# Kernel tuning notes

Measured on AMD Instinct MI355X. Metric: run time of the kernel, lower is better.

The kernel has to match this reference:

```python
import jax, jax.numpy as jnp
import numpy as np

B, L, HID, NH, E = 2, 2048, 1024, 16, 128
HS = HID // NH  # attention_head_size = 64 (scores scaled by sqrt(HS), NOT sqrt(E))


def setup_inputs() -> dict:
    key = jax.random.key(0)
    ks = jax.random.split(key, 8)
    s = 0.02
    return {
        "hidden_states": jax.random.normal(ks[0], (B, L, HID), jnp.float32),
        "attention_mask": jnp.zeros((B, 1, 1, L), jnp.float32),
        "rel_pos": jax.random.normal(ks[1], (1, NH, L, L), jnp.float32),
        "Wq": jax.random.normal(ks[2], (NH * E, HID), jnp.float32) * s,
        "bq": jnp.zeros((NH * E,), jnp.float32),
        "Wk": jax.random.normal(ks[3], (NH * E, HID), jnp.float32) * s,
        "Wv": jax.random.normal(ks[4], (HID, HID), jnp.float32) * s,
        "bv": jnp.zeros((HID,), jnp.float32),
        "Wg": jax.random.normal(ks[5], (8, E), jnp.float32) * s,
        "bg": jnp.zeros((8,), jnp.float32),
        "eco_a": jnp.ones((1, NH, 1, 1), jnp.float32),
    }


def reference(hidden_states, attention_mask, rel_pos, Wq, bq, Wk, Wv, bv, Wg, bg, eco_a):
    b, l, _ = hidden_states.shape
    # projections -> [B, H, L, E] / [B, H, L, HS]
    q = (hidden_states @ Wq.T + bq).reshape(b, l, NH, E).transpose(0, 2, 1, 3)
    k = (hidden_states @ Wk.T).reshape(b, l, NH, E).transpose(0, 2, 1, 3)
    v = (hidden_states @ Wv.T + bv).reshape(b, l, NH, HS).transpose(0, 2, 1, 3)
    scores = jnp.einsum('bhqe,bhke->bhqk', q, k) / jnp.asarray(np.sqrt(HS), q.dtype)
    scores = scores + attention_mask
    # gated relative-position bias: gate_ur_linear(q) -> [B,H,L,2,4] -> sum -> sigmoid
    g = jax.nn.sigmoid((q @ Wg.T + bg).reshape(b, NH, l, 2, 4).sum(-1))
    gate_u, gate_r = g[..., 0:1], g[..., 1:2]  # each [B,H,L,1]
    gate_u_1 = gate_u * (gate_r * eco_a - 1.0) + 2.0
    scores = scores + gate_u_1 * rel_pos
    probs = jax.nn.softmax(scores, axis=-1)  # dropout p=0 -> identity
    ctx = jnp.einsum('bhqk,bhkd->bhqd', probs, v)
    return ctx.transpose(0, 2, 1, 3).reshape(b, l, HID)
```

## Files before the change

### kernel.cpp

```cpp
#include <hip/hip_runtime.h>
#include <hip/hip_bf16.h>
#include <stdint.h>

#define Bn 2
#define Ln 2048
#define HIDn 1024
#define NHn 16
#define En 128
#define HSn 64

typedef unsigned short u16;
typedef short s16x8 __attribute__((ext_vector_type(8)));
typedef float f32x4 __attribute__((ext_vector_type(4)));
typedef float f32x16 __attribute__((ext_vector_type(16)));

__device__ __forceinline__ u16 f2bf(float f) {
  union { float f; uint32_t u; } v; v.f = f;
  uint32_t r = (v.u + 0x7fffu + ((v.u >> 16) & 1u)) >> 16;
  return (u16)r;
}
__device__ __forceinline__ float bf2f(u16 b) {
  union { uint32_t u; float f; } v; v.u = ((uint32_t)b) << 16;
  return v.f;
}
__device__ __forceinline__ void async16(const void* g, void* l) {
  __builtin_amdgcn_global_load_lds((const __attribute__((address_space(1))) void*)g,
                                   (__attribute__((address_space(3))) void*)l, 16, 0, 0);
}

__global__ void castbf(const float* __restrict__ in, u16* __restrict__ out, int n) {
  int i = (blockIdx.x * blockDim.x + threadIdx.x) * 4;
  if (i >= n) return;
  float4 v = *(const float4*)(in + i);
  u16 o[4] = {f2bf(v.x), f2bf(v.y), f2bf(v.z), f2bf(v.w)};
  *(uint64_t*)(out + i) = *(uint64_t*)o;
}

__global__ void wgprep(const float* __restrict__ Wg, float* __restrict__ wgu,
                       float* __restrict__ wgr) {
  int e = threadIdx.x;
  wgu[e] = Wg[0 * 128 + e] + Wg[1 * 128 + e] + Wg[2 * 128 + e] + Wg[3 * 128 + e];
  wgr[e] = Wg[4 * 128 + e] + Wg[5 * 128 + e] + Wg[6 * 128 + e] + Wg[7 * 128 + e];
}

__global__ __launch_bounds__(256) void qkv_gemm(
    const u16* __restrict__ A, const u16* __restrict__ W,
    const float* __restrict__ bq, const float* __restrict__ bv,
    u16* __restrict__ qb, u16* __restrict__ kb, u16* __restrict__ vt) {
  __shared__ union {
    struct { u16 a[128 * 32]; u16 b[128 * 32]; } st;
    u16 cq[64][140];
    u16 cv[128][72];
  } lds;
  const int tid = threadIdx.x, lane = tid & 63, w = tid >> 6;
  const int quad = lane >> 4, ln = lane & 15;
  const int bx = blockIdx.x, by = blockIdx.y;
  const int m0 = (w >> 1) * 64, n0 = (w & 1) * 64;
  f32x4 acc[4][4];
  for (int i = 0; i < 4; ++i)
    for (int j = 0; j < 4; ++j) acc[i][j] = (f32x4)0.0f;

  for (int k0 = 0; k0 < 1024; k0 += 32) {
    __syncthreads();
    for (int cc = 0; cc < 2; ++cc) {
      int c = w * 2 + cc;
      int row = c * 16 + (lane >> 2);
      int ke = (lane & 3) * 8;
      async16(A + (size_t)(by * 128 + row) * 1024 + k0 + ke, lds.st.a + c * 512);
      async16(W + (size_t)(bx * 128 + row) * 1024 + k0 + ke, lds.st.b + c * 512);
    }
    __syncthreads();
    s16x8 a[4], bf[4];
    for (int i = 0; i < 4; ++i)
      a[i] = *(const s16x8*)&lds.st.a[(m0 + i * 16 + ln) * 32 + quad * 8];
    for (int j = 0; j < 4; ++j)
      bf[j] = *(const s16x8*)&lds.st.b[(n0 + j * 16 + ln) * 32 + quad * 8];
    for (int i = 0; i < 4; ++i)
      for (int j = 0; j < 4; ++j)
        acc[i][j] = __builtin_amdgcn_mfma_f32_16x16x32_bf16(a[i], bf[j], acc[i][j], 0, 0, 0);
  }

  float bias[4];
#pragma unroll
  for (int j = 0; j < 4; ++j) {
    int col = bx * 128 + n0 + j * 16 + ln;
    bias[j] = (bx < 16) ? bq[col] : (bx >= 32 ? bv[col - 4096] : 0.0f);
  }

  if (bx < 32) {
    for (int half = 0; half < 2; ++half) {
      __syncthreads();
      if ((w >> 1) == half) {
#pragma unroll
        for (int i = 0; i < 4; ++i)
#pragma unroll
          for (int j = 0; j < 4; ++j)
#pragma unroll
            for (int r = 0; r < 4; ++r)
              lds.cq[i * 16 + quad * 4 + r][n0 + j * 16 + ln] = f2bf(acc[i][j][r] + bias[j]);
      }
      __syncthreads();
#pragma unroll
      for (int it = 0; it < 4; ++it) {
        int slot = it * 256 + tid;
        int row = slot >> 4, seg = slot & 15;
        int rowg = by * 128 + half * 64 + row;
        int b = rowg >> 11, l = rowg & 2047;
        uint4 d = *(const uint4*)&lds.cq[row][seg * 8];
        if (bx < 16) {
          *(uint4*)(qb + ((size_t)(b * 16 + bx) * 2048 + l) * 128 + seg * 8) = d;
        } else {
          int sg = (seg ^ (l & 15)) & 15;
          *(uint4*)(kb + ((size_t)(b * 16 + (bx - 16)) * 2048 + l) * 128 + sg * 8) = d;
        }
      }
    }
  } else {
    for (int half = 0; half < 2; ++half) {
      __syncthreads();
      if ((w >> 1) == half) {
#pragma unroll
        for (int i = 0; i < 4; ++i)
#pragma unroll
          for (int j = 0; j < 4; ++j)
#pragma unroll
            for (int r = 0; r < 4; ++r)
              lds.cv[n0 + j * 16 + ln][i * 16 + quad * 4 + r] = f2bf(acc[i][j][r] + bias[j]);
      }
      __syncthreads();
      int rowg = by * 128 + half * 64;
      int b = rowg >> 11, lbase = rowg & 2047;
#pragma unroll
      for (int it = 0; it < 4; ++it) {
        int slot = it * 256 + tid;
        int row = slot >> 3, seg = slot & 7;
        int c2 = (bx - 32) * 128 + row;
        int h = c2 >> 6, hs = c2 & 63;
        int sg = seg ^ (hs & 7);
        uint4 d = *(const uint4*)&lds.cv[row][seg * 8];
        *(uint4*)(vt + ((size_t)(b * 16 + h) * 64 + hs) * 2048 + lbase + sg * 8) = d;
      }
    }
  }
}

__global__ void gate_kernel(const u16* __restrict__ qb, const float* __restrict__ wgu,
                            const float* __restrict__ wgr, const float* __restrict__ bg,
                            const float* __restrict__ eco, float* __restrict__ gate) {
  int t = blockIdx.x * 256 + threadIdx.x;
  int h = (t >> 11) & 15;
  const u16* q = qb + (size_t)t * 128;
  float u = bg[0] + bg[1] + bg[2] + bg[3];
  float rr = bg[4] + bg[5] + bg[6] + bg[7];
  for (int e = 0; e < 128; e += 8) {
    uint4 d = *(const uint4*)(q + e);
    const u16* p = (const u16*)&d;
#pragma unroll
    for (int jj = 0; jj < 8; ++jj) {
      float f = bf2f(p[jj]);
      u += f * wgu[e + jj];
      rr += f * wgr[e + jj];
    }
  }
  float gu = 1.0f / (1.0f + __expf(-u));
  float gr = 1.0f / (1.0f + __expf(-rr));
  gate[t] = gu * (gr * eco[h] - 1.0f) + 2.0f;
}

__global__ __launch_bounds__(256, 2) void attn_kernel(
    const u16* __restrict__ qb, const u16* __restrict__ kbp, const u16* __restrict__ vt,
    const float* __restrict__ mask, const float* __restrict__ relpos,
    const float* __restrict__ gate, float* __restrict__ out) {
  __shared__ u16 sK[2][64 * 128];
  __shared__ u16 sVt[2][64 * 64];
  __shared__ float sRP[128 * 64];

  const int tid = threadIdx.x, lane = tid & 63, w = tid >> 6;
  const int q5 = lane & 31, hi = lane >> 5;
  const int bx = blockIdx.x, h = blockIdx.y;
  const int qt = bx >> 1, b = bx & 1;
  const int q0 = qt * 128;
  const u16* qptr = qb + (size_t)(b * NHn + h) * Ln * En;
  const u16* kptr = kbp + (size_t)(b * NHn + h) * Ln * En;
  const u16* vptr = vt + (size_t)(b * NHn + h) * HSn * Ln;
  const float* rpb = relpos + (size_t)h * Ln * Ln + (size_t)q0 * Ln;
  const float* mk = mask + (size_t)b * Ln;
  const float* gt = gate + (size_t)(b * NHn + h) * Ln;

  s16x8 aq[8];
  {
    const u16* qrow = qptr + (size_t)(q0 + w * 32 + q5) * En;
#pragma unroll
    for (int es = 0; es < 8; ++es)
      aq[es] = *(const s16x8*)(qrow + es * 16 + hi * 8);
  }
  const float gv = gt[q0 + w * 32 + q5];

  float l_part = 0.0f;
  f32x16 O0 = (f32x16)0.0f, O1 = (f32x16)0.0f;

  auto stage = [&](int buf, int kt) {
    const int kbase = kt * 64;
#pragma unroll
    for (int cc = 0; cc < 4; ++cc) {
      int c = w * 4 + cc;
      async16(kptr + (size_t)(kbase + c * 4 + (lane >> 4)) * En + (lane & 15) * 8,
              &sK[buf][c * 512]);
    }
#pragma unroll
    for (int cc = 0; cc < 2; ++cc) {
      int c = w * 2 + cc;
      async16(vptr + (size_t)(c * 8 + (lane >> 3)) * Ln + kbase + (lane & 7) * 8,
              &sVt[buf][c * 512]);
    }
  };
  auto rpload = [&](int kt, float4 (&rg)[8]) {
#pragma unroll
    for (int i = 0; i < 8; ++i) {
      int s = i * 256 + tid;
      int qq = s >> 4, gc = s & 15;
      rg[i] = *(const float4*)(rpb + (size_t)qq * Ln + kt * 64 + gc * 4);
    }
  };
  auto rpwrite = [&](const float4 (&rg)[8]) {
#pragma unroll
    for (int i = 0; i < 8; ++i) {
      int s = i * 256 + tid;
      int qq = s >> 4, gc = s & 15;
      *(float4*)&sRP[qq * 64 + ((gc ^ (qq & 15)) * 4)] = rg[i];
    }
  };

  const int NT = Ln / 64;
  stage(0, 0);
  float4 rg[8];
  rpload(0, rg);
  rpwrite(rg);

  for (int kt = 0; kt < NT; ++kt) {
    const int cur = kt & 1;
    __syncthreads();
    if (kt + 1 < NT) {
      stage(cur ^ 1, kt + 1);
      rpload(kt + 1, rg);
    }

    const u16* sKc = sK[cur];
    f32x16 S0 = (f32x16)0.0f, S1 = (f32x16)0.0f;
    __builtin_amdgcn_s_setprio(1);
#pragma unroll
    for (int es = 0; es < 8; ++es) {
      int gsw = ((es * 2 + hi) ^ (q5 & 15)) * 8;
      s16x8 ak0 = *(const s16x8*)&sKc[q5 * 128 + gsw];
      S0 = __builtin_amdgcn_mfma_f32_32x32x16_bf16(ak0, aq[es], S0, 0, 0, 0);
      s16x8 ak1 = *(const s16x8*)&sKc[(32 + q5) * 128 + gsw];
      S1 = __builtin_amdgcn_mfma_f32_32x32x16_bf16(ak1, aq[es], S1, 0, 0, 0);
    }
    __builtin_amdgcn_s_setprio(0);

    uint32_t pkv[16];
#pragma unroll
    for (int kbi = 0; kbi < 2; ++kbi) {
      const f32x16 Sa = kbi ? S1 : S0;
#pragma unroll
      for (int g = 0; g < 4; ++g) {
        f32x4 rp4 = *(const f32x4*)&sRP[(w * 32 + q5) * 64 +
                                        (((kbi * 8 + g * 2 + hi) ^ (q5 & 15)) * 4)];
        float4 mv4 = *(const float4*)(mk + kt * 64 + kbi * 32 + g * 8 + hi * 4);
        float p0 = __expf(fmaf(gv, rp4[0], fmaf(Sa[4 * g + 0], 0.125f, mv4.x)));
        float p1 = __expf(fmaf(gv, rp4[1], fmaf(Sa[4 * g + 1], 0.125f, mv4.y)));
        float p2 = __expf(fmaf(gv, rp4[2], fmaf(Sa[4 * g + 2], 0.125f, mv4.z)));
        float p3 = __expf(fmaf(gv, rp4[3], fmaf(Sa[4 * g + 3], 0.125f, mv4.w)));
        l_part += (p0 + p1) + (p2 + p3);
        uint32_t c0, c1;
        asm("v_cvt_pk_bf16_f32 %0, %1, %2" : "=v"(c0) : "v"(p0), "v"(p1));
        asm("v_cvt_pk_bf16_f32 %0, %1, %2" : "=v"(c1) : "v"(p2), "v"(p3));
        pkv[kbi * 8 + g * 2] = c0;
        pkv[kbi * 8 + g * 2 + 1] = c1;
      }
    }
#pragma unroll
    for (int base = 0; base < 16; base += 8) {
      asm volatile("v_permlane32_swap_b32 %0, %1" : "+v"(pkv[base + 0]), "+v"(pkv[base + 2]));
      asm volatile("v_permlane32_swap_b32 %0, %1" : "+v"(pkv[base + 1]), "+v"(pkv[base + 3]));
      asm volatile("v_permlane32_swap_b32 %0, %1" : "+v"(pkv[base + 4]), "+v"(pkv[base + 6]));
      asm volatile("v_permlane32_swap_b32 %0, %1" : "+v"(pkv[base + 5]), "+v"(pkv[base + 7]));
    }

    if (kt + 1 < NT) {
#pragma unroll
      for (int i = 0; i < 8; ++i)
        asm volatile("" : "+v"(rg[i].x), "+v"(rg[i].y), "+v"(rg[i].z), "+v"(rg[i].w));
    }
    __syncthreads();
    if (kt + 1 < NT) rpwrite(rg);

    const u16* sVc = sVt[cur];
    __builtin_amdgcn_s_setprio(1);
#pragma unroll
    for (int ks2 = 0; ks2 < 4; ++ks2) {
      union { uint32_t u[4]; s16x8 v; } pu;
      pu.u[0] = pkv[ks2 * 4 + 0];
      pu.u[1] = pkv[ks2 * 4 + 1];
      pu.u[2] = pkv[ks2 * 4 + 2];
      pu.u[3] = pkv[ks2 * 4 + 3];
      s16x8 pa = pu.v;
      int gsw = ((ks2 * 2 + hi) ^ (q5 & 7)) * 8;
      s16x8 bv0 = *(const s16x8*)&sVc[q5 * 64 + gsw];
      O0 = __builtin_amdgcn_mfma_f32_32x32x16_bf16(pa, bv0, O0, 0, 0, 0);
      s16x8 bv1 = *(const s16x8*)&sVc[(32 + q5) * 64 + gsw];
      O1 = __builtin_amdgcn_mfma_f32_32x32x16_bf16(pa, bv1, O1, 0, 0, 0);
    }
    __builtin_amdgcn_s_setprio(0);
  }

  float lt = l_part + __shfl_xor(l_part, 32, 64);
  float inv = 1.0f / lt;
#pragma unroll
  for (int i = 0; i < 16; ++i) {
    int qr = (i & 3) + 8 * (i >> 2) + 4 * hi;
    float iv = __shfl(inv, qr, 64);
    int qg = q0 + w * 32 + qr;
    float* orow = out + ((size_t)b * Ln + qg) * HIDn + h * 64;
    orow[q5] = O0[i] * iv;
    orow[32 + q5] = O1[i] * iv;
  }
}

extern "C" void kernel_launch(void* const* d_in, const int* in_sizes, int n_in,
                              void* d_out, int out_size, void* d_ws, size_t ws_size,
                              hipStream_t stream) {
  const float* hs = (const float*)d_in[0];
  const float* mask = (const float*)d_in[1];
  const float* relpos = (const float*)d_in[2];
  const float* Wq = (const float*)d_in[3];
  const float* bq = (const float*)d_in[4];
  const float* Wk = (const float*)d_in[5];
  const float* Wv = (const float*)d_in[6];
  const float* bv = (const float*)d_in[7];
  const float* Wg = (const float*)d_in[8];
  const float* bg = (const float*)d_in[9];
  const float* eco = (const float*)d_in[10];
  float* out = (float*)d_out;

  char* ws = (char*)d_ws;
  u16* hsb = (u16*)ws;
  u16* wb = (u16*)(ws + (8ull << 20));
  u16* qb = (u16*)(ws + (18ull << 20));
  u16* kb = (u16*)(ws + (34ull << 20));
  u16* vt = (u16*)(ws + (50ull << 20));
  float* gate = (float*)(ws + (58ull << 20));
  float* wgu = (float*)(ws + (58ull << 20) + (1ull << 19));
  float* wgr = wgu + 128;

  castbf<<<4096, 256, 0, stream>>>(hs, hsb, 4096 * 1024);
  castbf<<<2048, 256, 0, stream>>>(Wq, wb, 2048 * 1024);
  castbf<<<2048, 256, 0, stream>>>(Wk, wb + 2048 * 1024, 2048 * 1024);
  castbf<<<1024, 256, 0, stream>>>(Wv, wb + 4096 * 1024, 1024 * 1024);
  wgprep<<<1, 128, 0, stream>>>(Wg, wgu, wgr);
  qkv_gemm<<<dim3(40, 32), 256, 0, stream>>>(hsb, wb, bq, bv, qb, kb, vt);
  gate_kernel<<<256, 256, 0, stream>>>(qb, wgu, wgr, bg, eco, gate);
  attn_kernel<<<dim3(32, 16), 256, 0, stream>>>(qb, kb, vt, mask, relpos, gate, out);
}
```

Before: 551.0 us.

## Deepen K/V and rel_pos prefetch pipeline with explicit vmcnt waits and barriers

```diff
diff --git a/kernel.cpp b/kernel.cpp
--- a/kernel.cpp
+++ b/kernel.cpp
@@ -232,18 +232,17 @@
   };
 
   const int NT = Ln / 64;
-  stage(0, 0);
+  float mcons = mk[lane];
   float4 rg[8];
   rpload(0, rg);
+  stage(0, 0);
   rpwrite(rg);
+  rpload(1, rg);
+  stage(1, 1);
+  asm volatile("s_waitcnt vmcnt(14) lgkmcnt(0)\n\ts_barrier" ::: "memory");
 
   for (int kt = 0; kt < NT; ++kt) {
     const int cur = kt & 1;
-    __syncthreads();
-    if (kt + 1 < NT) {
-      stage(cur ^ 1, kt + 1);
-      rpload(kt + 1, rg);
-    }
 
     const u16* sKc = sK[cur];
     f32x16 S0 = (f32x16)0.0f, S1 = (f32x16)0.0f;
@@ -266,11 +265,15 @@
       for (int g = 0; g < 4; ++g) {
         f32x4 rp4 = *(const f32x4*)&sRP[(w * 32 + q5) * 64 +
                                         (((kbi * 8 + g * 2 + hi) ^ (q5 & 15)) * 4)];
-        float4 mv4 = *(const float4*)(mk + kt * 64 + kbi * 32 + g * 8 + hi * 4);
-        float p0 = __expf(fmaf(gv, rp4[0], fmaf(Sa[4 * g + 0], 0.125f, mv4.x)));
-        float p1 = __expf(fmaf(gv, rp4[1], fmaf(Sa[4 * g + 1], 0.125f, mv4.y)));
-        float p2 = __expf(fmaf(gv, rp4[2], fmaf(Sa[4 * g + 2], 0.125f, mv4.z)));
-        float p3 = __expf(fmaf(gv, rp4[3], fmaf(Sa[4 * g + 3], 0.125f, mv4.w)));
+        int mb = kbi * 32 + g * 8 + hi * 4;
+        float m0 = __shfl(mcons, mb + 0, 64);
+        float m1 = __shfl(mcons, mb + 1, 64);
+        float m2 = __shfl(mcons, mb + 2, 64);
+        float m3 = __shfl(mcons, mb + 3, 64);
+        float p0 = __expf(fmaf(gv, rp4[0], fmaf(Sa[4 * g + 0], 0.125f, m0)));
+        float p1 = __expf(fmaf(gv, rp4[1], fmaf(Sa[4 * g + 1], 0.125f, m1)));
+        float p2 = __expf(fmaf(gv, rp4[2], fmaf(Sa[4 * g + 2], 0.125f, m2)));
+        float p3 = __expf(fmaf(gv, rp4[3], fmaf(Sa[4 * g + 3], 0.125f, m3)));
         l_part += (p0 + p1) + (p2 + p3);
         uint32_t c0, c1;
         asm("v_cvt_pk_bf16_f32 %0, %1, %2" : "=v"(c0) : "v"(p0), "v"(p1));
@@ -287,13 +290,14 @@
       asm volatile("v_permlane32_swap_b32 %0, %1" : "+v"(pkv[base + 5]), "+v"(pkv[base + 7]));
     }
 
-    if (kt + 1 < NT) {
-#pragma unroll
-      for (int i = 0; i < 8; ++i)
-        asm volatile("" : "+v"(rg[i].x), "+v"(rg[i].y), "+v"(rg[i].z), "+v"(rg[i].w));
-    }
-    __syncthreads();
+    asm volatile("s_waitcnt vmcnt(6) lgkmcnt(0)\n\ts_barrier" ::: "memory");
     if (kt + 1 < NT) rpwrite(rg);
+    if (kt + 2 < NT) {
+      mcons = mk[(kt + 1) * 64 + lane];
+      rpload(kt + 2, rg);
+    } else if (kt + 1 < NT) {
+      mcons = mk[(kt + 1) * 64 + lane];
+    }
 
     const u16* sVc = sVt[cur];
     __builtin_amdgcn_s_setprio(1);
@@ -312,6 +316,13 @@
       O1 = __builtin_amdgcn_mfma_f32_32x32x16_bf16(pa, bv1, O1, 0, 0, 0);
     }
     __builtin_amdgcn_s_setprio(0);
+
+    if (kt + 2 < NT) {
+      asm volatile("s_waitcnt vmcnt(9) lgkmcnt(0)\n\ts_barrier" ::: "memory");
+      stage(cur, kt + 2);
+    } else {
+      asm volatile("s_waitcnt vmcnt(0) lgkmcnt(0)\n\ts_barrier" ::: "memory");
+    }
   }
 
   float lt = l_part + __shfl_xor(l_part, 32, 64);
```

After: 838.5 us. +52.2%, slower.
